# Performance work log

Measured on AMD Instinct MI355X. Metric: run time of the kernel, lower is better.

## Reference

```python
import jax, jax.numpy as jnp
import numpy as np

V, D, H, L, FF, NA, NB, S, C, BS = 32000, 768, 12, 6, 3072, 2, 2, 512, 10, 16
MOE_LAYERS = (1, 3, 5)
NE = NA * NB


def _ln(x, g, b, eps=1e-5):
    m = x.mean(-1, keepdims=True)
    v = ((x - m) ** 2).mean(-1, keepdims=True)
    return (x - m) / jnp.sqrt(v + eps) * g + b


def _ffn(x, W1, B1, W2, B2):
    # GLU-style FFN: w2(a * silu(b)) where [a, b] = chunk(w1(x), 2)
    h = x @ W1.T + B1
    a, b = jnp.split(h, 2, -1)
    return (a * jax.nn.silu(b)) @ W2.T + B2


def _mha(x, wqkv, bqkv, wo, bo):
    Bq, Sq, d = x.shape
    dh = d // H
    qkv = x @ wqkv.T + bqkv
    q, k, v = jnp.split(qkv, 3, -1)
    q = q.reshape(Bq, Sq, H, dh).transpose(0, 2, 1, 3)
    k = k.reshape(Bq, Sq, H, dh).transpose(0, 2, 1, 3)
    v = v.reshape(Bq, Sq, H, dh).transpose(0, 2, 1, 3)
    scores = jnp.einsum('bhqd,bhkd->bhqk', q, k) / jnp.sqrt(jnp.float32(dh))
    attn = jax.nn.softmax(scores, axis=-1)
    o = jnp.einsum('bhqk,bhkd->bhqd', attn, v)
    o = o.transpose(0, 2, 1, 3).reshape(Bq, Sq, d)
    return o @ wo.T + bo


def _moe(xf, W1, B1, W2, B2, gAw, gAb, gBw, gBb):
    pA = jax.nn.softmax(xf @ gAw.T + gAb, axis=-1)  # [T, NA]
    pB = jax.nn.softmax(xf @ gBw.T + gBb, axis=-1)  # [T, NB]
    iA = jnp.argmax(pA, -1)
    iB = jnp.argmax(pB, -1)
    auxA = NA * (pA.mean(0) * jax.nn.one_hot(iA, NA).mean(0)).sum()
    auxB = NB * (pB.mean(0) * jax.nn.one_hot(iB, NB).mean(0)).sum()
    e = iA * NB + iB  # [T] flattened expert id
    # dense all-expert compute then per-token select (E is small = 4)
    h = jnp.einsum('td,efd->etf', xf, W1) + B1[:, None, :]  # [NE, T, 2*FF]
    a, b = jnp.split(h, 2, -1)
    y = jnp.einsum('etf,edf->etd', a * jax.nn.silu(b), W2) + B2[:, None, :]
    out = y[e, jnp.arange(xf.shape[0])]  # [T, D]
    return out, auxA + auxB


def _forward(tok_emb, pos_emb, wqkv, bqkv, wo, bo, ln1g, ln1b, ln2g, ln2b,
             dW1, dB1, dW2, dB2, mW1, mB1, mW2, mB2, gAw, gAb, gBw, gBb,
             cW1, cB1, cW2, cB2, input_ids):
    x = tok_emb[input_ids] + pos_emb[None, :, :]
    total_aux = jnp.float32(0.0)
    di = mi = 0
    for l in range(L):
        x = _ln(x + _mha(x, wqkv[l], bqkv[l], wo[l], bo[l]), ln1g[l], ln1b[l])
        if l in MOE_LAYERS:
            xf = x.reshape(BS * S, D)
            f, aux = _moe(xf, mW1[mi], mB1[mi], mW2[mi], mB2[mi],
                          gAw[mi], gAb[mi], gBw[mi], gBb[mi])
            mi += 1
            total_aux = total_aux + aux
            f = f.reshape(BS, S, D)
        else:
            f = _ffn(x, dW1[di], dB1[di], dW2[di], dB2[di])
            di += 1
        x = _ln(x + f, ln2g[l], ln2b[l])
    rep = x.mean(1)  # mean pooling (no cls token / mask)
    hcls = jax.nn.relu(rep @ cW1.T + cB1)
    logits = hcls @ cW2.T + cB2
    return logits, total_aux


def setup_inputs() -> dict:
    key = jax.random.key(0)
    ks = iter(jax.random.split(key, 48))
    r = lambda shape, s=0.02: jax.random.normal(next(ks), shape, jnp.float32) * s
    Ld, Lm = L - len(MOE_LAYERS), len(MOE_LAYERS)
    return dict(
        input_ids=jax.random.randint(next(ks), (BS, S), 0, V),
        tok_emb=r((V, D)),
        pos_emb=r((S, D), 0.01),
        wqkv=r((L, 3 * D, D)), bqkv=jnp.zeros((L, 3 * D), jnp.float32),
        wo=r((L, D, D)), bo=jnp.zeros((L, D), jnp.float32),
        ln1g=jnp.ones((L, D), jnp.float32), ln1b=jnp.zeros((L, D), jnp.float32),
        ln2g=jnp.ones((L, D), jnp.float32), ln2b=jnp.zeros((L, D), jnp.float32),
        dW1=r((Ld, 2 * FF, D)), dB1=jnp.zeros((Ld, 2 * FF), jnp.float32),
        dW2=r((Ld, D, FF)), dB2=jnp.zeros((Ld, D), jnp.float32),
        mW1=r((Lm, NE, 2 * FF, D)), mB1=jnp.zeros((Lm, NE, 2 * FF), jnp.float32),
        mW2=r((Lm, NE, D, FF)), mB2=jnp.zeros((Lm, NE, D), jnp.float32),
        gAw=r((Lm, NA, D)), gAb=jnp.zeros((Lm, NA), jnp.float32),
        gBw=r((Lm, NB, D)), gBb=jnp.zeros((Lm, NB), jnp.float32),
        cW1=r((D, D)), cB1=jnp.zeros((D,), jnp.float32),
        cW2=r((C, D)), cB2=jnp.zeros((C,), jnp.float32),
    )


def reference(input_ids, tok_emb, pos_emb, wqkv, bqkv, wo, bo, ln1g, ln1b,
              ln2g, ln2b, dW1, dB1, dW2, dB2, mW1, mB1, mW2, mB2,
              gAw, gAb, gBw, gBb, cW1, cB1, cW2, cB2):
    return _forward(tok_emb, pos_emb, wqkv, bqkv, wo, bo, ln1g, ln1b, ln2g,
                    ln2b, dW1, dB1, dW2, dB2, mW1, mB1, mW2, mB2,
                    gAw, gAb, gBw, gBb, cW1, cB1, cW2, cB2, input_ids)
```

## Files before the change

### kernel.cpp

```cpp
#include <hip/hip_runtime.h>
#include <cstddef>

#define TOK   8192
#define DIMD  768
#define NH    12
#define DHD   64
#define SEQ   512
#define NB_   16
#define FFD   3072
#define NEXP  4
#define CCLS  10
#define FF2   (2*FFD)

typedef short bf16x8 __attribute__((ext_vector_type(8)));
typedef float f32x4  __attribute__((ext_vector_type(4)));

static const size_t OFF_X    = 0;
static const size_t OFF_XB   = OFF_X   + (size_t)TOK*DIMD;
static const size_t OFF_F    = OFF_XB  + (size_t)TOK*DIMD/2;
static const size_t OFF_SH   = OFF_F   + (size_t)TOK*DIMD;
static const size_t SH_FL    = (size_t)8704*FF2/2;
static const size_t OFF_WQ   = OFF_SH  + SH_FL;
static const size_t OFF_WOB  = OFF_WQ  + (size_t)3*DIMD*DIMD/2;
static const size_t OFF_W1B  = OFF_WOB + (size_t)DIMD*DIMD/2;
static const size_t OFF_W2B  = OFF_W1B + (size_t)NEXP*FF2*DIMD/2;
static const size_t OFF_REP  = OFF_W2B + (size_t)NEXP*DIMD*FFD/2;
static const size_t OFF_HCLS = OFF_REP + (size_t)NB_*DIMD;
static const size_t OFF_STAT = OFF_HCLS+ (size_t)NB_*DIMD;
static const size_t OFF_INT  = OFF_STAT+ 8;
static const size_t OFF_AUX  = OFF_INT + 160;
static const size_t OFF_EID  = OFF_AUX + 1;
static const size_t OFF_PERM = OFF_EID + TOK;

__device__ __forceinline__ ushort f2bf(float f) {
    union { float f; unsigned u; } v; v.f = f;
    unsigned r = v.u + 0x7FFF + ((v.u >> 16) & 1);
    return (ushort)(r >> 16);
}
__device__ __forceinline__ float bf2f(ushort u) {
    union { unsigned u; float f; } v; v.u = ((unsigned)u) << 16;
    return v.f;
}
__device__ __forceinline__ void gload16(const void* g, void* l) {
    __builtin_amdgcn_global_load_lds((const __attribute__((address_space(1))) void*)g,
                                     (__attribute__((address_space(3))) void*)l, 16, 0, 0);
}
__device__ __forceinline__ uint4 glu8(uint4 a8, uint4 b8) {
    const ushort* ap = (const ushort*)&a8;
    const ushort* bp = (const ushort*)&b8;
    ushort r[8];
#pragma unroll
    for (int j = 0; j < 8; ++j) {
        float a = bf2f(ap[j]), b = bf2f(bp[j]);
        r[j] = f2bf(a * (b / (1.f + __expf(-b))));
    }
    return *(uint4*)r;
}

__global__ __launch_bounds__(256) void k_cvt(const float* __restrict__ s, ushort* __restrict__ d, int n8)
{
    int i = blockIdx.x * 256 + threadIdx.x;
    if (i >= n8) return;
    float4 x0 = ((const float4*)s)[i * 2];
    float4 x1 = ((const float4*)s)[i * 2 + 1];
    ushort r[8] = { f2bf(x0.x), f2bf(x0.y), f2bf(x0.z), f2bf(x0.w),
                    f2bf(x1.x), f2bf(x1.y), f2bf(x1.z), f2bf(x1.w) };
    ((uint4*)d)[i] = *(uint4*)r;
}

__global__ __launch_bounds__(256) void k_embed(const int* __restrict__ ids,
                                               const float* __restrict__ te,
                                               const float* __restrict__ pe,
                                               float* __restrict__ x,
                                               ushort* __restrict__ xb)
{
    int i = blockIdx.x * 256 + threadIdx.x;
    const int nd4 = DIMD / 4;
    if (i >= TOK * nd4) return;
    int t = i / nd4, d4 = i % nd4;
    int s = t % SEQ;
    int id = ids[t];
    float4 a = ((const float4*)(te + (size_t)id * DIMD))[d4];
    float4 b = ((const float4*)(pe + (size_t)s  * DIMD))[d4];
    float4 o; o.x = a.x + b.x; o.y = a.y + b.y; o.z = a.z + b.z; o.w = a.w + b.w;
    ((float4*)(x + (size_t)t * DIMD))[d4] = o;
    ushort4 ob = make_ushort4(f2bf(o.x), f2bf(o.y), f2bf(o.z), f2bf(o.w));
    *(ushort4*)(xb + (size_t)t * DIMD + d4 * 4) = ob;
}

template<int GATHER, int GLUA, int CBF, int SCAT>
__global__ __launch_bounds__(256) void k_mm(const ushort* __restrict__ A,
                                            const ushort* __restrict__ Wb,
                                            const float* __restrict__ bias,
                                            void* __restrict__ C_,
                                            int N, int K,
                                            const int* __restrict__ perm,
                                            const int* __restrict__ offs,
                                            const int* __restrict__ blke,
                                            const int* __restrict__ blkb,
                                            const int* __restrict__ nblk)
{
    constexpr int MOE = GATHER || SCAT;
    __shared__ ushort As[2][128 * 32];
    __shared__ ushort Bs[2][128 * 32];
    __shared__ int    toks[128];
    const int tid = threadIdx.x, lane = tid & 63, w = tid >> 6;
    const int rb = blockIdx.y;
    const int n0 = blockIdx.x * 128;
    const int row0 = rb * 128;
    const ushort* W = Wb;
    const float*  bi = bias;
    int lb = 0, cnt = 1 << 30;
    if constexpr (MOE) {
        if (rb >= *nblk) return;
        int e = blke[rb];
        lb = blkb[rb];
        int base = offs[e];
        cnt = offs[e + 1] - base;
        W  += (size_t)e * N * K;
        bi += (size_t)e * N;
        if (tid < 128) { int rg = lb + tid; toks[tid] = perm[base + (rg < cnt ? rg : cnt - 1)]; }
        __syncthreads();
    }
    const int sr = lane >> 2;
    const int sc = (lane & 3) * 8;
    int ar0, ar1;
    if constexpr (GATHER) { ar0 = toks[w * 16 + sr]; ar1 = toks[64 + w * 16 + sr]; }
    else                  { ar0 = row0 + w * 16 + sr; ar1 = row0 + 64 + w * 16 + sr; }
    const int br0 = n0 + w * 16 + sr, br1 = n0 + 64 + w * 16 + sr;
    const int gsr = tid >> 2;
    const int gsc = (tid & 3) * 8;

    const int l15 = lane & 15, l4 = lane >> 4;
    const int wm = w >> 1, wn = w & 1;
    f32x4 acc[4][4] = {};

    if constexpr (!GLUA) {
        gload16(A + (size_t)ar0 * K + sc, &As[0][(w * 16) * 32]);
        gload16(A + (size_t)ar1 * K + sc, &As[0][(64 + w * 16) * 32]);
    } else {
        uint4 a0 = *(const uint4*)(A + (size_t)(row0 + gsr) * 2 * K + gsc);
        uint4 b0 = *(const uint4*)(A + (size_t)(row0 + gsr) * 2 * K + K + gsc);
        uint4 a1 = *(const uint4*)(A + (size_t)(row0 + 64 + gsr) * 2 * K + gsc);
        uint4 b1 = *(const uint4*)(A + (size_t)(row0 + 64 + gsr) * 2 * K + K + gsc);
        *(uint4*)&As[0][gsr * 32 + gsc]        = glu8(a0, b0);
        *(uint4*)&As[0][(64 + gsr) * 32 + gsc] = glu8(a1, b1);
    }
    gload16(W + (size_t)br0 * K + sc, &Bs[0][(w * 16) * 32]);
    gload16(W + (size_t)br1 * K + sc, &Bs[0][(64 + w * 16) * 32]);
    __syncthreads();

    int cur = 0;
    const int NT = K / 32;
    for (int t = 0; t < NT; ++t) {
        const int nk = (t + 1) * 32;
        uint4 ga0, gb0, ga1, gb1;
        if (t + 1 < NT) {
            if constexpr (!GLUA) {
                gload16(A + (size_t)ar0 * K + nk + sc, &As[cur ^ 1][(w * 16) * 32]);
                gload16(A + (size_t)ar1 * K + nk + sc, &As[cur ^ 1][(64 + w * 16) * 32]);
            } else {
                ga0 = *(const uint4*)(A + (size_t)(row0 + gsr) * 2 * K + nk + gsc);
                gb0 = *(const uint4*)(A + (size_t)(row0 + gsr) * 2 * K + K + nk + gsc);
                ga1 = *(const uint4*)(A + (size_t)(row0 + 64 + gsr) * 2 * K + nk + gsc);
                gb1 = *(const uint4*)(A + (size_t)(row0 + 64 + gsr) * 2 * K + K + nk + gsc);
            }
            gload16(W + (size_t)br0 * K + nk + sc, &Bs[cur ^ 1][(w * 16) * 32]);
            gload16(W + (size_t)br1 * K + nk + sc, &Bs[cur ^ 1][(64 + w * 16) * 32]);
        }
        bf16x8 af[4], bf_[4];
#pragma unroll
        for (int i = 0; i < 4; ++i) {
            af[i]  = *(const bf16x8*)&As[cur][(wm * 64 + i * 16 + l15) * 32 + l4 * 8];
            bf_[i] = *(const bf16x8*)&Bs[cur][(wn * 64 + i * 16 + l15) * 32 + l4 * 8];
        }
#pragma unroll
        for (int mi = 0; mi < 4; ++mi)
#pragma unroll
            for (int ni = 0; ni < 4; ++ni)
                acc[mi][ni] = __builtin_amdgcn_mfma_f32_16x16x32_bf16(af[mi], bf_[ni], acc[mi][ni], 0, 0, 0);
        if (t + 1 < NT) {
            if constexpr (GLUA) {
                *(uint4*)&As[cur ^ 1][gsr * 32 + gsc]        = glu8(ga0, gb0);
                *(uint4*)&As[cur ^ 1][(64 + gsr) * 32 + gsc] = glu8(ga1, gb1);
            }
        }
        __syncthreads();
        cur ^= 1;
    }
#pragma unroll
    for (int ni = 0; ni < 4; ++ni) {
        int col = n0 + wn * 64 + ni * 16 + l15;
        float bb = bi[col];
#pragma unroll
        for (int mi = 0; mi < 4; ++mi) {
            int ri = wm * 64 + mi * 16 + l4 * 4;
#pragma unroll
            for (int r = 0; r < 4; ++r) {
                float o = acc[mi][ni][r] + bb;
                if constexpr (SCAT) {
                    if (lb + ri + r < cnt)
                        ((float*)C_)[(size_t)toks[ri + r] * N + col] = o;
                } else if constexpr (CBF) {
                    ((ushort*)C_)[(size_t)(row0 + ri + r) * N + col] = f2bf(o);
                } else {
                    ((float*)C_)[(size_t)(row0 + ri + r) * N + col] = o;
                }
            }
        }
    }
}

__global__ __launch_bounds__(256) void k_attn(const ushort* __restrict__ qkv, ushort* __restrict__ out)
{
    __shared__ ushort Qs[64][72];
    __shared__ ushort Ks[64][72];
    __shared__ ushort Vt[64][72];
    __shared__ ushort Ps[4][16][72];
    const int bh = blockIdx.x;
    const int b = bh / NH, h = bh % NH;
    const int qt = blockIdx.y;
    const int tid = threadIdx.x, lane = tid & 63, w = tid >> 6;
    const int l15 = lane & 15, l4 = lane >> 4;
    const int t0 = b * SEQ + qt * 64;
    {
        int r = tid >> 3, c8 = (tid & 7) * 8;
#pragma unroll
        for (int p = 0; p < 2; ++p) {
            int rr = r + p * 32;
            *(uint4*)&Qs[rr][c8] = *(const uint4*)(qkv + (size_t)(t0 + rr) * 3 * DIMD + h * DHD + c8);
        }
    }
    __syncthreads();
    bf16x8 aq[2];
    aq[0] = *(const bf16x8*)&Qs[w*16 + l15][l4*8];
    aq[1] = *(const bf16x8*)&Qs[w*16 + l15][32 + l4*8];
    f32x4 o[4] = {};
    float m[4], lsum[4];
#pragma unroll
    for (int r = 0; r < 4; ++r) { m[r] = -3.0e38f; lsum[r] = 0.f; }
    for (int kt = 0; kt < SEQ; kt += 64) {
        __syncthreads();
        {
            int r = tid >> 3, c8 = (tid & 7) * 8;
#pragma unroll
            for (int p = 0; p < 2; ++p) {
                int rr = r + p * 32;
                const ushort* kp = qkv + (size_t)(b * SEQ + kt + rr) * 3 * DIMD + DIMD + h * DHD;
                *(uint4*)&Ks[rr][c8] = *(const uint4*)(kp + c8);
                uint4 vv = *(const uint4*)(kp + DIMD + c8);
                const ushort* vs = (const ushort*)&vv;
#pragma unroll
                for (int j = 0; j < 8; ++j) Vt[c8 + j][rr] = vs[j];
            }
        }
        __syncthreads();
        f32x4 s[4] = {};
#pragma unroll
        for (int kk = 0; kk < 2; ++kk)
#pragma unroll
            for (int ni = 0; ni < 4; ++ni) {
                bf16x8 bk = *(const bf16x8*)&Ks[ni*16 + l15][kk*32 + l4*8];
                s[ni] = __builtin_amdgcn_mfma_f32_16x16x32_bf16(aq[kk], bk, s[ni], 0, 0, 0);
            }
        float csc[4];
#pragma unroll
        for (int r = 0; r < 4; ++r) {
            float mx = -3.0e38f;
#pragma unroll
            for (int ni = 0; ni < 4; ++ni) { s[ni][r] *= 0.125f; mx = fmaxf(mx, s[ni][r]); }
            mx = fmaxf(mx, __shfl_xor(mx, 1));
            mx = fmaxf(mx, __shfl_xor(mx, 2));
            mx = fmaxf(mx, __shfl_xor(mx, 4));
            mx = fmaxf(mx, __shfl_xor(mx, 8));
            float nm = fmaxf(m[r], mx);
            float c = __expf(m[r] - nm);
            m[r] = nm;
            float ps = 0.f;
#pragma unroll
            for (int ni = 0; ni < 4; ++ni) { s[ni][r] = __expf(s[ni][r] - nm); ps += s[ni][r]; }
            ps += __shfl_xor(ps, 1);
            ps += __shfl_xor(ps, 2);
            ps += __shfl_xor(ps, 4);
            ps += __shfl_xor(ps, 8);
            lsum[r] = lsum[r] * c + ps;
            csc[r] = c;
#pragma unroll
            for (int ni = 0; ni < 4; ++ni)
                Ps[w][l4*4 + r][ni*16 + l15] = f2bf(s[ni][r]);
        }
#pragma unroll
        for (int di = 0; di < 4; ++di)
#pragma unroll
            for (int r = 0; r < 4; ++r) o[di][r] *= csc[r];
        bf16x8 ap[2];
        ap[0] = *(const bf16x8*)&Ps[w][l15][l4*8];
        ap[1] = *(const bf16x8*)&Ps[w][l15][32 + l4*8];
#pragma unroll
        for (int kk = 0; kk < 2; ++kk)
#pragma unroll
            for (int di = 0; di < 4; ++di) {
                bf16x8 bv = *(const bf16x8*)&Vt[di*16 + l15][kk*32 + l4*8];
                o[di] = __builtin_amdgcn_mfma_f32_16x16x32_bf16(ap[kk], bv, o[di], 0, 0, 0);
            }
    }
    float inv[4];
#pragma unroll
    for (int r = 0; r < 4; ++r) inv[r] = 1.f / lsum[r];
#pragma unroll
    for (int di = 0; di < 4; ++di)
#pragma unroll
        for (int r = 0; r < 4; ++r)
            out[(size_t)(t0 + w*16 + l4*4 + r) * DIMD + h * DHD + di*16 + l15] = f2bf(o[di][r] * inv[r]);
}

__global__ __launch_bounds__(256) void k_ln(float* __restrict__ x, const float* __restrict__ f,
                                            const float* __restrict__ g, const float* __restrict__ b,
                                            ushort* __restrict__ xb)
{
    const int t = blockIdx.x, tid = threadIdx.x;
    __shared__ float y[DIMD];
    __shared__ float red[256];
    float* xr = x + (size_t)t * DIMD;
    const float* fr = f + (size_t)t * DIMD;
    float s = 0.f;
    for (int d = tid; d < DIMD; d += 256) { float v = xr[d] + fr[d]; y[d] = v; s += v; }
    red[tid] = s; __syncthreads();
    for (int off = 128; off > 0; off >>= 1) { if (tid < off) red[tid] += red[tid + off]; __syncthreads(); }
    const float mean = red[0] * (1.f / DIMD);
    __syncthreads();
    s = 0.f;
    for (int d = tid; d < DIMD; d += 256) { float v = y[d] - mean; s += v * v; }
    red[tid] = s; __syncthreads();
    for (int off = 128; off > 0; off >>= 1) { if (tid < off) red[tid] += red[tid + off]; __syncthreads(); }
    const float rstd = 1.f / sqrtf(red[0] * (1.f / DIMD) + 1e-5f);
    for (int d = tid; d < DIMD; d += 256) {
        float v = (y[d] - mean) * rstd * g[d] + b[d];
        xr[d] = v;
        xb[(size_t)t * DIMD + d] = f2bf(v);
    }
}

__global__ __launch_bounds__(256) void k_gate(const float* __restrict__ x,
                                              const float* __restrict__ gAw, const float* __restrict__ gAb,
                                              const float* __restrict__ gBw, const float* __restrict__ gBb,
                                              float* __restrict__ sums, int* __restrict__ cnts,
                                              int* __restrict__ e_id)
{
    const int tid = threadIdx.x, lane = tid & 63, wid = tid >> 6;
    const int gw = blockIdx.x * 4 + wid;
    float wA0[12], wA1[12], wB0[12], wB1[12];
#pragma unroll
    for (int i = 0; i < 12; ++i) {
        int d = lane + i * 64;
        wA0[i] = gAw[d]; wA1[i] = gAw[DIMD + d];
        wB0[i] = gBw[d]; wB1[i] = gBw[DIMD + d];
    }
    const float bA0 = gAb[0], bA1 = gAb[1], bB0 = gBb[0], bB1 = gBb[1];
    float sA0 = 0.f, sA1 = 0.f, sB0 = 0.f, sB1 = 0.f;
    int cA1 = 0, cB1 = 0, cE0 = 0, cE1 = 0, cE2 = 0;
    for (int i = 0; i < 32; ++i) {
        int t = gw * 32 + i;
        const float* xr = x + (size_t)t * DIMD;
        float a0 = 0.f, a1 = 0.f, b0 = 0.f, b1 = 0.f;
#pragma unroll
        for (int j = 0; j < 12; ++j) {
            float v = xr[lane + j * 64];
            a0 = fmaf(v, wA0[j], a0); a1 = fmaf(v, wA1[j], a1);
            b0 = fmaf(v, wB0[j], b0); b1 = fmaf(v, wB1[j], b1);
        }
#pragma unroll
        for (int off = 1; off < 64; off <<= 1) {
            a0 += __shfl_xor(a0, off); a1 += __shfl_xor(a1, off);
            b0 += __shfl_xor(b0, off); b1 += __shfl_xor(b1, off);
        }
        a0 += bA0; a1 += bA1; b0 += bB0; b1 += bB1;
        int iA = (a1 > a0) ? 1 : 0;
        int iB = (b1 > b0) ? 1 : 0;
        float mA = fmaxf(a0, a1); float eA0 = __expf(a0 - mA), eA1 = __expf(a1 - mA);
        float dA = 1.f / (eA0 + eA1);
        float mB = fmaxf(b0, b1); float eB0 = __expf(b0 - mB), eB1 = __expf(b1 - mB);
        float dB = 1.f / (eB0 + eB1);
        sA0 += eA0 * dA; sA1 += eA1 * dA;
        sB0 += eB0 * dB; sB1 += eB1 * dB;
        cA1 += iA; cB1 += iB;
        int e = iA * 2 + iB;
        cE0 += (e == 0); cE1 += (e == 1); cE2 += (e == 2);
        if (lane == 0) e_id[t] = e;
    }
    __shared__ float fpart[4][4];
    __shared__ int   ipart[4][8];
    if (lane == 0) {
        fpart[wid][0] = sA0; fpart[wid][1] = sA1; fpart[wid][2] = sB0; fpart[wid][3] = sB1;
        ipart[wid][0] = 32 - cA1; ipart[wid][1] = cA1;
        ipart[wid][2] = 32 - cB1; ipart[wid][3] = cB1;
        ipart[wid][4] = cE0; ipart[wid][5] = cE1; ipart[wid][6] = cE2;
        ipart[wid][7] = 32 - cE0 - cE1 - cE2;
    }
    __syncthreads();
    if (tid < 4)  atomicAdd(sums + tid, fpart[0][tid] + fpart[1][tid] + fpart[2][tid] + fpart[3][tid]);
    else if (tid >= 64 && tid < 72) {
        int k = tid - 64;
        atomicAdd(cnts + k, ipart[0][k] + ipart[1][k] + ipart[2][k] + ipart[3][k]);
    }
}

__global__ void k_offsets(const int* __restrict__ cntE, int* __restrict__ offs, int* __restrict__ cursor,
                          int* __restrict__ nblk, int* __restrict__ blke, int* __restrict__ blkb)
{
    if (threadIdx.x == 0) {
        int a = 0, nb = 0;
        for (int e = 0; e < NEXP; ++e) {
            offs[e] = a; a += cntE[e]; cursor[e] = 0;
            int blocks = (cntE[e] + 127) >> 7;
            for (int b = 0; b < blocks; ++b) { blke[nb] = e; blkb[nb] = b * 128; ++nb; }
        }
        offs[NEXP] = a;
        *nblk = nb;
    }
}

__global__ __launch_bounds__(256) void k_scatter(const int* __restrict__ e_id, const int* __restrict__ offs,
                                                 int* __restrict__ cursor, int* __restrict__ perm)
{
    int t = blockIdx.x * 256 + threadIdx.x;
    int lane = threadIdx.x & 63;
    int e = e_id[t];
#pragma unroll
    for (int eo = 0; eo < NEXP; ++eo) {
        unsigned long long m = __ballot(e == eo);
        if (m == 0ULL) continue;
        int leader = __ffsll((long long)m) - 1;
        int base = 0;
        if (lane == leader) base = atomicAdd(cursor + eo, (int)__popcll(m));
        base = __shfl(base, leader);
        if (e == eo) {
            int lower = (int)__popcll(m & ((1ULL << lane) - 1ULL));
            perm[offs[eo] + base + lower] = t;
        }
    }
}

__global__ void k_aux(const float* __restrict__ sums, const int* __restrict__ cnts, float* __restrict__ aux_acc)
{
    if (threadIdx.x == 0) {
        const float invT2 = 1.f / ((float)TOK * (float)TOK);
        float aA = 2.f * (sums[0] * (float)cnts[0] + sums[1] * (float)cnts[1]) * invT2;
        float aB = 2.f * (sums[2] * (float)cnts[2] + sums[3] * (float)cnts[3]) * invT2;
        *aux_acc += aA + aB;
    }
}

__global__ __launch_bounds__(256) void k_rep(const float* __restrict__ x, float* __restrict__ rep)
{
    int i = blockIdx.x * 256 + threadIdx.x;
    if (i >= NB_ * DIMD) return;
    int b = i / DIMD, d = i % DIMD;
    float s = 0.f;
    for (int q = 0; q < SEQ; ++q) s += x[((size_t)b * SEQ + q) * DIMD + d];
    rep[i] = s * (1.f / SEQ);
}

__global__ __launch_bounds__(256) void k_cls1(const float* __restrict__ rep, const float* __restrict__ cW1,
                                              const float* __restrict__ cB1, float* __restrict__ hcls)
{
    int w = blockIdx.x * 4 + (threadIdx.x >> 6);
    int lane = threadIdx.x & 63;
    if (w >= NB_ * DIMD) return;
    int b = w / DIMD, i = w % DIMD;
    float s = 0.f;
    for (int d = lane; d < DIMD; d += 64) s += rep[b * DIMD + d] * cW1[(size_t)i * DIMD + d];
    for (int off = 32; off > 0; off >>= 1) s += __shfl_down(s, off);
    if (lane == 0) hcls[w] = fmaxf(s + cB1[i], 0.f);
}

__global__ __launch_bounds__(256) void k_cls2(const float* __restrict__ hcls, const float* __restrict__ cW2,
                                              const float* __restrict__ cB2, float* __restrict__ out)
{
    int w = blockIdx.x * 4 + (threadIdx.x >> 6);
    int lane = threadIdx.x & 63;
    if (w >= NB_ * CCLS) return;
    int b = w / CCLS, c = w % CCLS;
    float s = 0.f;
    for (int d = lane; d < DIMD; d += 64) s += hcls[b * DIMD + d] * cW2[(size_t)c * DIMD + d];
    for (int off = 32; off > 0; off >>= 1) s += __shfl_down(s, off);
    if (lane == 0) out[w] = s + cB2[c];
}

__global__ void k_writeaux(const float* __restrict__ aux_acc, float* __restrict__ out)
{
    if (threadIdx.x == 0) out[NB_ * CCLS] = *aux_acc;
}

extern "C" void kernel_launch(void* const* d_in, const int* in_sizes, int n_in,
                              void* d_out, int out_size, void* d_ws, size_t ws_size,
                              hipStream_t stream)
{
    const int*   input_ids = (const int*)  d_in[0];
    const float* tok_emb   = (const float*)d_in[1];
    const float* pos_emb   = (const float*)d_in[2];
    const float* wqkv      = (const float*)d_in[3];
    const float* bqkv      = (const float*)d_in[4];
    const float* wo        = (const float*)d_in[5];
    const float* bo        = (const float*)d_in[6];
    const float* ln1g      = (const float*)d_in[7];
    const float* ln1b      = (const float*)d_in[8];
    const float* ln2g      = (const float*)d_in[9];
    const float* ln2b      = (const float*)d_in[10];
    const float* dW1       = (const float*)d_in[11];
    const float* dB1       = (const float*)d_in[12];
    const float* dW2       = (const float*)d_in[13];
    const float* dB2       = (const float*)d_in[14];
    const float* mW1       = (const float*)d_in[15];
    const float* mB1       = (const float*)d_in[16];
    const float* mW2       = (const float*)d_in[17];
    const float* mB2       = (const float*)d_in[18];
    const float* gAw       = (const float*)d_in[19];
    const float* gAb       = (const float*)d_in[20];
    const float* gBw       = (const float*)d_in[21];
    const float* gBb       = (const float*)d_in[22];
    const float* cW1       = (const float*)d_in[23];
    const float* cB1       = (const float*)d_in[24];
    const float* cW2       = (const float*)d_in[25];
    const float* cB2       = (const float*)d_in[26];

    float* out = (float*)d_out;
    float* ws  = (float*)d_ws;

    float*  X    = ws + OFF_X;
    ushort* XB   = (ushort*)(ws + OFF_XB);
    float*  F    = ws + OFF_F;
    ushort* QKV  = (ushort*)(ws + OFF_SH);
    ushort* G    = (ushort*)(ws + OFF_SH + (size_t)TOK * 3 * DIMD / 2);
    ushort* Hh   = (ushort*)(ws + OFF_SH);
    ushort* WQB  = (ushort*)(ws + OFF_WQ);
    ushort* WOB  = (ushort*)(ws + OFF_WOB);
    ushort* W1B  = (ushort*)(ws + OFF_W1B);
    ushort* W2B  = (ushort*)(ws + OFF_W2B);
    float*  REP  = ws + OFF_REP;
    float*  HCLS = ws + OFF_HCLS;
    float*  SUMS = ws + OFF_STAT;
    int*    INTB = (int*)(ws + OFF_INT);
    int*    CNTS = INTB;
    int*    OFFS = INTB + 8;
    int*    CURS = INTB + 13;
    int*    NBLK = INTB + 17;
    int*    BLKE = INTB + 18;
    int*    BLKB = INTB + 86;
    float*  AUXP = ws + OFF_AUX;
    int*    EID  = (int*)(ws + OFF_EID);
    int*    PERM = (int*)(ws + OFF_PERM);

    hipMemsetAsync(AUXP, 0, sizeof(float), stream);

    k_embed<<<dim3((TOK * DIMD / 4) / 256), 256, 0, stream>>>(input_ids, tok_emb, pos_emb, X, XB);

    int di = 0, mi = 0;
    for (int l = 0; l < 6; ++l) {
        const int moe = (l == 1 || l == 3 || l == 5);
        {
            int n8 = 3 * DIMD * DIMD / 8;
            k_cvt<<<dim3((n8 + 255) / 256), 256, 0, stream>>>(wqkv + (size_t)l * 3 * DIMD * DIMD, WQB, n8);
            n8 = DIMD * DIMD / 8;
            k_cvt<<<dim3((n8 + 255) / 256), 256, 0, stream>>>(wo + (size_t)l * DIMD * DIMD, WOB, n8);
            if (moe) {
                n8 = NEXP * FF2 * DIMD / 8;
                k_cvt<<<dim3((n8 + 255) / 256), 256, 0, stream>>>(mW1 + (size_t)mi * NEXP * FF2 * DIMD, W1B, n8);
                n8 = NEXP * DIMD * FFD / 8;
                k_cvt<<<dim3((n8 + 255) / 256), 256, 0, stream>>>(mW2 + (size_t)mi * NEXP * DIMD * FFD, W2B, n8);
            } else {
                n8 = FF2 * DIMD / 8;
                k_cvt<<<dim3((n8 + 255) / 256), 256, 0, stream>>>(dW1 + (size_t)di * FF2 * DIMD, W1B, n8);
                n8 = DIMD * FFD / 8;
                k_cvt<<<dim3((n8 + 255) / 256), 256, 0, stream>>>(dW2 + (size_t)di * DIMD * FFD, W2B, n8);
            }
        }
        k_mm<0,0,1,0><<<dim3(3 * DIMD / 128, TOK / 128), 256, 0, stream>>>(
            XB, WQB, bqkv + (size_t)l * 3 * DIMD, QKV, 3 * DIMD, DIMD,
            nullptr, nullptr, nullptr, nullptr, nullptr);
        k_attn<<<dim3(NB_ * NH, SEQ / 64), 256, 0, stream>>>(QKV, G);
        k_mm<0,0,0,0><<<dim3(DIMD / 128, TOK / 128), 256, 0, stream>>>(
            G, WOB, bo + (size_t)l * DIMD, F, DIMD, DIMD,
            nullptr, nullptr, nullptr, nullptr, nullptr);
        k_ln<<<TOK, 256, 0, stream>>>(X, F, ln1g + (size_t)l * DIMD, ln1b + (size_t)l * DIMD, XB);

        if (moe) {
            hipMemsetAsync(SUMS, 0, 64, stream);
            k_gate<<<64, 256, 0, stream>>>(X,
                gAw + (size_t)mi * 2 * DIMD, gAb + (size_t)mi * 2,
                gBw + (size_t)mi * 2 * DIMD, gBb + (size_t)mi * 2,
                SUMS, CNTS, EID);
            k_offsets<<<1, 1, 0, stream>>>(CNTS + 4, OFFS, CURS, NBLK, BLKE, BLKB);
            k_scatter<<<TOK / 256, 256, 0, stream>>>(EID, OFFS, CURS, PERM);
            k_mm<1,0,1,0><<<dim3(FF2 / 128, 67), 256, 0, stream>>>(
                XB, W1B, mB1 + (size_t)mi * NEXP * FF2, Hh, FF2, DIMD,
                PERM, OFFS, BLKE, BLKB, NBLK);
            k_mm<0,1,0,1><<<dim3(DIMD / 128, 67), 256, 0, stream>>>(
                Hh, W2B, mB2 + (size_t)mi * NEXP * DIMD, F, DIMD, FFD,
                PERM, OFFS, BLKE, BLKB, NBLK);
            k_aux<<<1, 1, 0, stream>>>(SUMS, CNTS, AUXP);
            ++mi;
        } else {
            k_mm<0,0,1,0><<<dim3(FF2 / 128, TOK / 128), 256, 0, stream>>>(
                XB, W1B, dB1 + (size_t)di * FF2, Hh, FF2, DIMD,
                nullptr, nullptr, nullptr, nullptr, nullptr);
            k_mm<0,1,0,0><<<dim3(DIMD / 128, TOK / 128), 256, 0, stream>>>(
                Hh, W2B, dB2 + (size_t)di * DIMD, F, DIMD, FFD,
                nullptr, nullptr, nullptr, nullptr, nullptr);
            ++di;
        }
        k_ln<<<TOK, 256, 0, stream>>>(X, F, ln2g + (size_t)l * DIMD, ln2b + (size_t)l * DIMD, XB);
    }

    k_rep<<<dim3((NB_ * DIMD + 255) / 256), 256, 0, stream>>>(X, REP);
    k_cls1<<<dim3(NB_ * DIMD / 4), 256, 0, stream>>>(REP, cW1, cB1, HCLS);
    k_cls2<<<dim3((NB_ * CCLS + 3) / 4), 256, 0, stream>>>(HCLS, cW2, cB2, out);
    k_writeaux<<<1, 1, 0, stream>>>(AUXP, out);
}
```

Measured before the change: 3.193 ms.

## Split GLU into in-place pass, re-layout LDS tiles, and remap blocks across XCDs

```diff
diff --git a/kernel.cpp b/kernel.cpp
--- a/kernel.cpp
+++ b/kernel.cpp
@@ -45,17 +45,6 @@
     __builtin_amdgcn_global_load_lds((const __attribute__((address_space(1))) void*)g,
                                      (__attribute__((address_space(3))) void*)l, 16, 0, 0);
 }
-__device__ __forceinline__ uint4 glu8(uint4 a8, uint4 b8) {
-    const ushort* ap = (const ushort*)&a8;
-    const ushort* bp = (const ushort*)&b8;
-    ushort r[8];
-#pragma unroll
-    for (int j = 0; j < 8; ++j) {
-        float a = bf2f(ap[j]), b = bf2f(bp[j]);
-        r[j] = f2bf(a * (b / (1.f + __expf(-b))));
-    }
-    return *(uint4*)r;
-}
 
 __global__ __launch_bounds__(256) void k_cvt(const float* __restrict__ s, ushort* __restrict__ d, int n8)
 {
@@ -88,12 +77,31 @@
     *(ushort4*)(xb + (size_t)t * DIMD + d4 * 4) = ob;
 }
 
-template<int GATHER, int GLUA, int CBF, int SCAT>
+__global__ __launch_bounds__(256) void k_gluip(ushort* __restrict__ h)
+{
+    int i = blockIdx.x * 256 + threadIdx.x;
+    const int nf8 = FFD / 8;
+    int row = i / nf8, j8 = i % nf8;
+    size_t base = (size_t)row * FF2 + j8 * 8;
+    uint4 a8 = *(const uint4*)(h + base);
+    uint4 b8 = *(const uint4*)(h + base + FFD);
+    const ushort* ap = (const ushort*)&a8;
+    const ushort* bp = (const ushort*)&b8;
+    ushort r[8];
+#pragma unroll
+    for (int j = 0; j < 8; ++j) {
+        float a = bf2f(ap[j]), b = bf2f(bp[j]);
+        r[j] = f2bf(a * (b / (1.f + __expf(-b))));
+    }
+    *(uint4*)(h + base) = *(uint4*)r;
+}
+
+template<int GATHER, int CBF, int SCAT>
 __global__ __launch_bounds__(256) void k_mm(const ushort* __restrict__ A,
                                             const ushort* __restrict__ Wb,
                                             const float* __restrict__ bias,
                                             void* __restrict__ C_,
-                                            int N, int K,
+                                            int N, int K, int lda,
                                             const int* __restrict__ perm,
                                             const int* __restrict__ offs,
                                             const int* __restrict__ blke,
@@ -101,20 +109,26 @@
                                             const int* __restrict__ nblk)
 {
     constexpr int MOE = GATHER || SCAT;
-    __shared__ ushort As[2][128 * 32];
-    __shared__ ushort Bs[2][128 * 32];
+    __shared__ ushort As[2][4096];
+    __shared__ ushort Bs[2][4096];
     __shared__ int    toks[128];
     const int tid = threadIdx.x, lane = tid & 63, w = tid >> 6;
-    const int rb = blockIdx.y;
-    const int n0 = blockIdx.x * 128;
-    const int row0 = rb * 128;
+    {
+    }
+    int bid = blockIdx.y * gridDim.x + blockIdx.x;
+    int nwg = gridDim.x * gridDim.y;
+    int q = nwg >> 3, r8 = nwg & 7;
+    int xcd = bid & 7, loc = bid >> 3;
+    int lbid = (xcd < r8 ? xcd * (q + 1) : r8 * (q + 1) + (xcd - r8) * q) + loc;
+    const int bx = lbid % gridDim.x, by = lbid / gridDim.x;
+    const int n0 = bx * 128, row0 = by * 128;
     const ushort* W = Wb;
     const float*  bi = bias;
     int lb = 0, cnt = 1 << 30;
     if constexpr (MOE) {
-        if (rb >= *nblk) return;
-        int e = blke[rb];
-        lb = blkb[rb];
+        if (by >= *nblk) return;
+        int e = blke[by];
+        lb = blkb[by];
         int base = offs[e];
         cnt = offs[e + 1] - base;
         W  += (size_t)e * N * K;
@@ -122,69 +136,45 @@
         if (tid < 128) { int rg = lb + tid; toks[tid] = perm[base + (rg < cnt ? rg : cnt - 1)]; }
         __syncthreads();
     }
-    const int sr = lane >> 2;
-    const int sc = (lane & 3) * 8;
     int ar0, ar1;
-    if constexpr (GATHER) { ar0 = toks[w * 16 + sr]; ar1 = toks[64 + w * 16 + sr]; }
-    else                  { ar0 = row0 + w * 16 + sr; ar1 = row0 + 64 + w * 16 + sr; }
-    const int br0 = n0 + w * 16 + sr, br1 = n0 + 64 + w * 16 + sr;
-    const int gsr = tid >> 2;
-    const int gsc = (tid & 3) * 8;
+    if constexpr (GATHER) { ar0 = toks[lane]; ar1 = toks[64 + lane]; }
+    else                  { ar0 = row0 + lane; ar1 = row0 + 64 + lane; }
+    const ushort* ap0 = A + (size_t)ar0 * lda + w * 8;
+    const ushort* ap1 = A + (size_t)ar1 * lda + w * 8;
+    const ushort* bp0 = W + (size_t)(n0 + lane) * K + w * 8;
+    const ushort* bp1 = W + (size_t)(n0 + 64 + lane) * K + w * 8;
 
     const int l15 = lane & 15, l4 = lane >> 4;
     const int wm = w >> 1, wn = w & 1;
     f32x4 acc[4][4] = {};
 
-    if constexpr (!GLUA) {
-        gload16(A + (size_t)ar0 * K + sc, &As[0][(w * 16) * 32]);
-        gload16(A + (size_t)ar1 * K + sc, &As[0][(64 + w * 16) * 32]);
-    } else {
-        uint4 a0 = *(const uint4*)(A + (size_t)(row0 + gsr) * 2 * K + gsc);
-        uint4 b0 = *(const uint4*)(A + (size_t)(row0 + gsr) * 2 * K + K + gsc);
-        uint4 a1 = *(const uint4*)(A + (size_t)(row0 + 64 + gsr) * 2 * K + gsc);
-        uint4 b1 = *(const uint4*)(A + (size_t)(row0 + 64 + gsr) * 2 * K + K + gsc);
-        *(uint4*)&As[0][gsr * 32 + gsc]        = glu8(a0, b0);
-        *(uint4*)&As[0][(64 + gsr) * 32 + gsc] = glu8(a1, b1);
-    }
-    gload16(W + (size_t)br0 * K + sc, &Bs[0][(w * 16) * 32]);
-    gload16(W + (size_t)br1 * K + sc, &Bs[0][(64 + w * 16) * 32]);
+    gload16(ap0, &As[0][w * 1024]);
+    gload16(ap1, &As[0][w * 1024 + 512]);
+    gload16(bp0, &Bs[0][w * 1024]);
+    gload16(bp1, &Bs[0][w * 1024 + 512]);
     __syncthreads();
 
+    const int NT = K / 32;
     int cur = 0;
-    const int NT = K / 32;
     for (int t = 0; t < NT; ++t) {
-        const int nk = (t + 1) * 32;
-        uint4 ga0, gb0, ga1, gb1;
         if (t + 1 < NT) {
-            if constexpr (!GLUA) {
-                gload16(A + (size_t)ar0 * K + nk + sc, &As[cur ^ 1][(w * 16) * 32]);
-                gload16(A + (size_t)ar1 * K + nk + sc, &As[cur ^ 1][(64 + w * 16) * 32]);
-            } else {
-                ga0 = *(const uint4*)(A + (size_t)(row0 + gsr) * 2 * K + nk + gsc);
-                gb0 = *(const uint4*)(A + (size_t)(row0 + gsr) * 2 * K + K + nk + gsc);
-                ga1 = *(const uint4*)(A + (size_t)(row0 + 64 + gsr) * 2 * K + nk + gsc);
-                gb1 = *(const uint4*)(A + (size_t)(row0 + 64 + gsr) * 2 * K + K + nk + gsc);
-            }
-            gload16(W + (size_t)br0 * K + nk + sc, &Bs[cur ^ 1][(w * 16) * 32]);
-            gload16(W + (size_t)br1 * K + nk + sc, &Bs[cur ^ 1][(64 + w * 16) * 32]);
+            int ko = (t + 1) * 32;
+            gload16(ap0 + ko, &As[cur ^ 1][w * 1024]);
+            gload16(ap1 + ko, &As[cur ^ 1][w * 1024 + 512]);
+            gload16(bp0 + ko, &Bs[cur ^ 1][w * 1024]);
+            gload16(bp1 + ko, &Bs[cur ^ 1][w * 1024 + 512]);
         }
         bf16x8 af[4], bf_[4];
 #pragma unroll
         for (int i = 0; i < 4; ++i) {
-            af[i]  = *(const bf16x8*)&As[cur][(wm * 64 + i * 16 + l15) * 32 + l4 * 8];
-            bf_[i] = *(const bf16x8*)&Bs[cur][(wn * 64 + i * 16 + l15) * 32 + l4 * 8];
+            af[i]  = *(const bf16x8*)&As[cur][l4 * 1024 + (wm * 64 + i * 16 + l15) * 8];
+            bf_[i] = *(const bf16x8*)&Bs[cur][l4 * 1024 + (wn * 64 + i * 16 + l15) * 8];
         }
 #pragma unroll
         for (int mi = 0; mi < 4; ++mi)
 #pragma unroll
             for (int ni = 0; ni < 4; ++ni)
                 acc[mi][ni] = __builtin_amdgcn_mfma_f32_16x16x32_bf16(af[mi], bf_[ni], acc[mi][ni], 0, 0, 0);
-        if (t + 1 < NT) {
-            if constexpr (GLUA) {
-                *(uint4*)&As[cur ^ 1][gsr * 32 + gsc]        = glu8(ga0, gb0);
-                *(uint4*)&As[cur ^ 1][(64 + gsr) * 32 + gsc] = glu8(ga1, gb1);
-            }
-        }
         __syncthreads();
         cur ^= 1;
     }
@@ -575,12 +565,12 @@
                 k_cvt<<<dim3((n8 + 255) / 256), 256, 0, stream>>>(dW2 + (size_t)di * DIMD * FFD, W2B, n8);
             }
         }
-        k_mm<0,0,1,0><<<dim3(3 * DIMD / 128, TOK / 128), 256, 0, stream>>>(
-            XB, WQB, bqkv + (size_t)l * 3 * DIMD, QKV, 3 * DIMD, DIMD,
+        k_mm<0,1,0><<<dim3(3 * DIMD / 128, TOK / 128), 256, 0, stream>>>(
+            XB, WQB, bqkv + (size_t)l * 3 * DIMD, QKV, 3 * DIMD, DIMD, DIMD,
             nullptr, nullptr, nullptr, nullptr, nullptr);
         k_attn<<<dim3(NB_ * NH, SEQ / 64), 256, 0, stream>>>(QKV, G);
-        k_mm<0,0,0,0><<<dim3(DIMD / 128, TOK / 128), 256, 0, stream>>>(
-            G, WOB, bo + (size_t)l * DIMD, F, DIMD, DIMD,
+        k_mm<0,0,0><<<dim3(DIMD / 128, TOK / 128), 256, 0, stream>>>(
+            G, WOB, bo + (size_t)l * DIMD, F, DIMD, DIMD, DIMD,
             nullptr, nullptr, nullptr, nullptr, nullptr);
         k_ln<<<TOK, 256, 0, stream>>>(X, F, ln1g + (size_t)l * DIMD, ln1b + (size_t)l * DIMD, XB);
 
@@ -592,20 +582,22 @@
                 SUMS, CNTS, EID);
             k_offsets<<<1, 1, 0, stream>>>(CNTS + 4, OFFS, CURS, NBLK, BLKE, BLKB);
             k_scatter<<<TOK / 256, 256, 0, stream>>>(EID, OFFS, CURS, PERM);
-            k_mm<1,0,1,0><<<dim3(FF2 / 128, 67), 256, 0, stream>>>(
-                XB, W1B, mB1 + (size_t)mi * NEXP * FF2, Hh, FF2, DIMD,
+            k_mm<1,1,0><<<dim3(FF2 / 128, 68), 256, 0, stream>>>(
+                XB, W1B, mB1 + (size_t)mi * NEXP * FF2, Hh, FF2, DIMD, DIMD,
                 PERM, OFFS, BLKE, BLKB, NBLK);
-            k_mm<0,1,0,1><<<dim3(DIMD / 128, 67), 256, 0, stream>>>(
-                Hh, W2B, mB2 + (size_t)mi * NEXP * DIMD, F, DIMD, FFD,
+            k_gluip<<<dim3(8704 * (FFD / 8) / 256), 256, 0, stream>>>(Hh);
+            k_mm<0,0,1><<<dim3(DIMD / 128, 68), 256, 0, stream>>>(
+                Hh, W2B, mB2 + (size_t)mi * NEXP * DIMD, F, DIMD, FFD, FF2,
                 PERM, OFFS, BLKE, BLKB, NBLK);
             k_aux<<<1, 1, 0, stream>>>(SUMS, CNTS, AUXP);
             ++mi;
         } else {
-            k_mm<0,0,1,0><<<dim3(FF2 / 128, TOK / 128), 256, 0, stream>>>(
-                XB, W1B, dB1 + (size_t)di * FF2, Hh, FF2, DIMD,
+            k_mm<0,1,0><<<dim3(FF2 / 128, TOK / 128), 256, 0, stream>>>(
+                XB, W1B, dB1 + (size_t)di * FF2, Hh, FF2, DIMD, DIMD,
                 nullptr, nullptr, nullptr, nullptr, nullptr);
-            k_mm<0,1,0,0><<<dim3(DIMD / 128, TOK / 128), 256, 0, stream>>>(
-                Hh, W2B, dB2 + (size_t)di * DIMD, F, DIMD, FFD,
+            k_gluip<<<dim3(8704 * (FFD / 8) / 256), 256, 0, stream>>>(Hh);
+            k_mm<0,0,0><<<dim3(DIMD / 128, TOK / 128), 256, 0, stream>>>(
+                Hh, W2B, dB2 + (size_t)di * DIMD, F, DIMD, FFD, FF2,
                 nullptr, nullptr, nullptr, nullptr, nullptr);
             ++di;
         }
```

Measured after the change: 3.359 ms. 1.05x slower.
